# Kernel tuning notes

Measured on AMD Instinct MI355X. Metric: run time of the kernel, lower is better.

Reference implementation:

```python
import jax, jax.numpy as jnp
from jax import lax
import numpy as np

SMOOTH = 0.015
EPS = 1e-9


def setup_inputs() -> dict:
    key = jax.random.key(0)
    k_x, k_a, k_p, k_b = jax.random.split(key, 4)
    B, F, T, C = 64, 256, 2048, 1
    x = jax.random.uniform(k_x, (B, F, T, C), dtype=jnp.float32)  # nonneg energies
    # learned scalars ~ N(1.0, 0.1) as in tf.random_normal_initializer(mean=1.0, stddev=0.1)
    alpha = 1.0 + 0.1 * jax.random.normal(k_a, (1,), dtype=jnp.float32)
    power = 1.0 + 0.1 * jax.random.normal(k_p, (1,), dtype=jnp.float32)
    bias = 1.0 + 0.1 * jax.random.normal(k_b, (1,), dtype=jnp.float32)
    return {"x": x, "alpha": alpha, "power": power, "bias": bias}


def _smoother(x):
    # x: [B, F, T, C]; IIR: M_0 = s*x_0, M_t = (1-s)*M_{t-1} + s*x_t
    xt = jnp.moveaxis(x, 2, 0)  # [T, B, F, C]
    m0 = SMOOTH * xt[0]

    def step(m_prev, xi):
        m = (1.0 - SMOOTH) * m_prev + SMOOTH * xi
        return m, m

    _, ms = lax.scan(step, m0, xt[1:])
    M = jnp.concatenate([m0[None], ms], axis=0)  # [T, B, F, C]
    return jnp.moveaxis(M, 0, 2)  # [B, F, T, C]


def reference(x, alpha, power, bias):
    M = _smoother(x)
    return jnp.power(x / jnp.power(EPS + M, alpha) + bias, power) - jnp.power(bias, power)
```

## Files before the change

kernel.cpp:

```cpp
#include <hip/hip_runtime.h>


#define T_LEN      2048
#define PAD_STRIDE 33
#define LDS_ROW    (64 * PAD_STRIDE)

__device__ __forceinline__ float fast_exp2(float x) { return __builtin_amdgcn_exp2f(x); }
__device__ __forceinline__ float fast_log2(float x) { return __builtin_amdgcn_logf(x); }

__global__ __launch_bounds__(256) void pcen_kernel(
    const float* __restrict__ x,
    const float* __restrict__ alpha_p,
    const float* __restrict__ power_p,
    const float* __restrict__ bias_p,
    float* __restrict__ out)
{
    __shared__ float lds[4][LDS_ROW];

    const int wave = threadIdx.x >> 6;
    const int lane = threadIdx.x & 63;
    const int row  = (blockIdx.x << 2) | wave;

    const float alpha = alpha_p[0];
    const float power = power_p[0];
    const float bias  = bias_p[0];

    const float A = 0.985f;
    const float S = 0.015f;

    const float* xr  = x   + (size_t)row * T_LEN;
    float*       orw = out + (size_t)row * T_LEN;
    float*       L   = lds[wave];

#pragma unroll
    for (int k = 0; k < 8; ++k) {
        const int e = 4 * lane + 256 * k;
        const float4 v = *reinterpret_cast<const float4*>(xr + e);
        const int idx = ((e >> 5) * PAD_STRIDE) + (e & 31);
        L[idx + 0] = v.x; L[idx + 1] = v.y; L[idx + 2] = v.z; L[idx + 3] = v.w;
    }
    __syncthreads();

    float xv[32], mv[32];
    const int base = lane * PAD_STRIDE;
    float m = 0.0f;
#pragma unroll
    for (int j = 0; j < 32; ++j) {
        const float xx = L[base + j];
        xv[j] = xx;
        m = A * m + S * xx;
        mv[j] = m;
    }

    float f = A; f *= f; f *= f; f *= f; f *= f; f *= f;
    float s = m;
    float g = f;
#pragma unroll
    for (int d = 1; d < 64; d <<= 1) {
        const float so = __shfl_up(s, d, 64);
        if (lane >= d) s += g * so;
        g *= g;
    }
    float carry = __shfl_up(s, 1, 64);
    if (lane == 0) carry = 0.0f;

    const float bias_pow = fast_exp2(power * fast_log2(bias));
    float pa = A * carry;
#pragma unroll
    for (int j = 0; j < 32; ++j) {
        const float M   = mv[j] + pa;
        pa *= A;
        const float den = 1e-9f + M;
        const float t   = xv[j] * fast_exp2(-alpha * fast_log2(den)) + bias;
        const float r   = fast_exp2(power * fast_log2(t)) - bias_pow;
        L[base + j] = r;
    }
    __syncthreads();

#pragma unroll
    for (int k = 0; k < 8; ++k) {
        const int e   = 4 * lane + 256 * k;
        const int idx = ((e >> 5) * PAD_STRIDE) + (e & 31);
        float4 v;
        v.x = L[idx + 0]; v.y = L[idx + 1]; v.z = L[idx + 2]; v.w = L[idx + 3];
        *reinterpret_cast<float4*>(orw + e) = v;
    }
}

extern "C" void kernel_launch(void* const* d_in, const int* in_sizes, int n_in,
                              void* d_out, int out_size, void* d_ws, size_t ws_size,
                              hipStream_t stream) {
    const float* x       = (const float*)d_in[0];
    const float* alpha_p = (const float*)d_in[1];
    const float* power_p = (const float*)d_in[2];
    const float* bias_p  = (const float*)d_in[3];
    float* out           = (float*)d_out;

    const int nrows  = in_sizes[0] / T_LEN;
    const int blocks = nrows / 4;

    pcen_kernel<<<blocks, 256, 0, stream>>>(x, alpha_p, power_p, bias_p, out);
}
```

Measured before the change: 237.8 us.

## Replace LDS transpose with chunked register scan and cross-chunk carry

Drops the shared-memory transpose. Each lane now loads 8 contiguous elements per 512-element chunk straight into registers, runs a local recurrence, then a wave-wide shuffle scan with a carry passed between four chunks. Later chunks are prefetched while earlier ones are computed. This removes the LDS traffic and the block barriers and lowers register pressure, allowing higher occupancy (launch bounds 256,8). The cost is more shuffle-scan rounds, four scans instead of one, and narrower per-lane memory accesses.

```diff
diff --git a/kernel.cpp b/kernel.cpp
--- a/kernel.cpp
+++ b/kernel.cpp
@@ -1,22 +1,20 @@
 #include <hip/hip_runtime.h>
 
 
-#define T_LEN      2048
-#define PAD_STRIDE 33
-#define LDS_ROW    (64 * PAD_STRIDE)
+#define T_LEN 2048
+#define CHUNK 512
+#define PLANE 8
 
 __device__ __forceinline__ float fast_exp2(float x) { return __builtin_amdgcn_exp2f(x); }
 __device__ __forceinline__ float fast_log2(float x) { return __builtin_amdgcn_logf(x); }
 
-__global__ __launch_bounds__(256) void pcen_kernel(
+__global__ __launch_bounds__(256, 8) void pcen_kernel(
     const float* __restrict__ x,
     const float* __restrict__ alpha_p,
     const float* __restrict__ power_p,
     const float* __restrict__ bias_p,
     float* __restrict__ out)
 {
-    __shared__ float lds[4][LDS_ROW];
-
     const int wave = threadIdx.x >> 6;
     const int lane = threadIdx.x & 63;
     const int row  = (blockIdx.x << 2) | wave;
@@ -27,64 +25,69 @@
 
     const float A = 0.985f;
     const float S = 0.015f;
+    float f8 = A * A; f8 *= f8; f8 *= f8;
 
-    const float* xr  = x   + (size_t)row * T_LEN;
-    float*       orw = out + (size_t)row * T_LEN;
-    float*       L   = lds[wave];
-
-#pragma unroll
-    for (int k = 0; k < 8; ++k) {
-        const int e = 4 * lane + 256 * k;
-        const float4 v = *reinterpret_cast<const float4*>(xr + e);
-        const int idx = ((e >> 5) * PAD_STRIDE) + (e & 31);
-        L[idx + 0] = v.x; L[idx + 1] = v.y; L[idx + 2] = v.z; L[idx + 3] = v.w;
-    }
-    __syncthreads();
-
-    float xv[32], mv[32];
-    const int base = lane * PAD_STRIDE;
-    float m = 0.0f;
-#pragma unroll
-    for (int j = 0; j < 32; ++j) {
-        const float xx = L[base + j];
-        xv[j] = xx;
-        m = A * m + S * xx;
-        mv[j] = m;
-    }
-
-    float f = A; f *= f; f *= f; f *= f; f *= f; f *= f;
-    float s = m;
-    float g = f;
-#pragma unroll
-    for (int d = 1; d < 64; d <<= 1) {
-        const float so = __shfl_up(s, d, 64);
-        if (lane >= d) s += g * so;
-        g *= g;
-    }
-    float carry = __shfl_up(s, 1, 64);
-    if (lane == 0) carry = 0.0f;
+    const float* xr  = x   + (size_t)row * T_LEN + PLANE * lane;
+    float*       orw = out + (size_t)row * T_LEN + PLANE * lane;
 
     const float bias_pow = fast_exp2(power * fast_log2(bias));
-    float pa = A * carry;
-#pragma unroll
-    for (int j = 0; j < 32; ++j) {
-        const float M   = mv[j] + pa;
-        pa *= A;
-        const float den = 1e-9f + M;
-        const float t   = xv[j] * fast_exp2(-alpha * fast_log2(den)) + bias;
-        const float r   = fast_exp2(power * fast_log2(t)) - bias_pow;
-        L[base + j] = r;
-    }
-    __syncthreads();
+    const float nalpha   = -alpha;
 
-#pragma unroll
-    for (int k = 0; k < 8; ++k) {
-        const int e   = 4 * lane + 256 * k;
-        const int idx = ((e >> 5) * PAD_STRIDE) + (e & 31);
-        float4 v;
-        v.x = L[idx + 0]; v.y = L[idx + 1]; v.z = L[idx + 2]; v.w = L[idx + 3];
-        *reinterpret_cast<float4*>(orw + e) = v;
-    }
+    float carry = 0.0f;
+
+    float4 a0 = *reinterpret_cast<const float4*>(xr + 0 * CHUNK);
+    float4 b0 = *reinterpret_cast<const float4*>(xr + 0 * CHUNK + 4);
+    float4 a1 = *reinterpret_cast<const float4*>(xr + 1 * CHUNK);
+    float4 b1 = *reinterpret_cast<const float4*>(xr + 1 * CHUNK + 4);
+    float4 a2, b2, a3, b3;
+
+#define PROC(cc, va, vb)                                                      \
+  {                                                                           \
+    float xv[PLANE];                                                          \
+    xv[0] = va.x; xv[1] = va.y; xv[2] = va.z; xv[3] = va.w;                   \
+    xv[4] = vb.x; xv[5] = vb.y; xv[6] = vb.z; xv[7] = vb.w;                   \
+    float mv[PLANE];                                                          \
+    float m = 0.0f;                                                           \
+    _Pragma("unroll")                                                         \
+    for (int j = 0; j < PLANE; ++j) { m = A * m + S * xv[j]; mv[j] = m; }     \
+    \
+    \
+    float s = (lane == 0) ? fmaf(f8, carry, m) : m;                           \
+    float g = f8;                                                             \
+    _Pragma("unroll")                                                         \
+    for (int d = 1; d < 64; d <<= 1) {                                        \
+      float so = __shfl_up(s, d, 64);                                         \
+      if (lane >= d) s = fmaf(g, so, s);                                      \
+      g *= g;                                                                 \
+    }                                                                         \
+    float C = __shfl_up(s, 1, 64);     \
+    if (lane == 0) C = carry;                                                 \
+    carry = __shfl(s, 63, 64);          \
+    float pa = A * C;                         \
+    _Pragma("unroll")                                                         \
+    for (int j = 0; j < PLANE; ++j) {                                         \
+      float M   = mv[j] + pa;                                                 \
+      pa *= A;                                                                \
+      float den = 1e-9f + M;                                                  \
+      float t   = fmaf(xv[j], fast_exp2(nalpha * fast_log2(den)), bias);      \
+      xv[j]     = fast_exp2(power * fast_log2(t)) - bias_pow;                 \
+    }                                                                         \
+    float4 w0, w1;                                                            \
+    w0.x = xv[0]; w0.y = xv[1]; w0.z = xv[2]; w0.w = xv[3];                   \
+    w1.x = xv[4]; w1.y = xv[5]; w1.z = xv[6]; w1.w = xv[7];                   \
+    *reinterpret_cast<float4*>(orw + (cc) * CHUNK)     = w0;                  \
+    *reinterpret_cast<float4*>(orw + (cc) * CHUNK + 4) = w1;                  \
+  }
+
+    a2 = *reinterpret_cast<const float4*>(xr + 2 * CHUNK);
+    b2 = *reinterpret_cast<const float4*>(xr + 2 * CHUNK + 4);
+    PROC(0, a0, b0);
+    a3 = *reinterpret_cast<const float4*>(xr + 3 * CHUNK);
+    b3 = *reinterpret_cast<const float4*>(xr + 3 * CHUNK + 4);
+    PROC(1, a1, b1);
+    PROC(2, a2, b2);
+    PROC(3, a3, b3);
+#undef PROC
 }
 
 extern "C" void kernel_launch(void* const* d_in, const int* in_sizes, int n_in,
```

New measurement: 237.2 us. Within noise of the previous version (-0.2%).

## Replace LDS transpose with register-resident chunked scan using cross-chunk carries

Applied to the files above, without the earlier changes.

Drops the shared-memory transpose and the two block barriers. Each lane now keeps its eight float4 loads in registers and runs eight interleaved 64-lane shuffle scans, one per 256-element chunk. Chunks are stitched together with a running carry read from lane 63. This removes LDS traffic and synchronisation, at the cost of more shuffle instructions (eight scans instead of one) and higher register pressure, with an occupancy hint added to the launch bounds.

```diff
diff --git a/kernel.cpp b/kernel.cpp
--- a/kernel.cpp
+++ b/kernel.cpp
@@ -1,22 +1,23 @@
 #include <hip/hip_runtime.h>
 
 
-#define T_LEN      2048
-#define PAD_STRIDE 33
-#define LDS_ROW    (64 * PAD_STRIDE)
+#define T_LEN 2048
+#define NCH   8
+#define CHUNK 256
 
 __device__ __forceinline__ float fast_exp2(float x) { return __builtin_amdgcn_exp2f(x); }
 __device__ __forceinline__ float fast_log2(float x) { return __builtin_amdgcn_logf(x); }
+__device__ __forceinline__ float readlane63(float v) {
+    return __int_as_float(__builtin_amdgcn_readlane(__float_as_int(v), 63));
+}
 
-__global__ __launch_bounds__(256) void pcen_kernel(
+__global__ __launch_bounds__(256, 4) void pcen_kernel(
     const float* __restrict__ x,
     const float* __restrict__ alpha_p,
     const float* __restrict__ power_p,
     const float* __restrict__ bias_p,
     float* __restrict__ out)
 {
-    __shared__ float lds[4][LDS_ROW];
-
     const int wave = threadIdx.x >> 6;
     const int lane = threadIdx.x & 63;
     const int row  = (blockIdx.x << 2) | wave;
@@ -27,63 +28,79 @@
 
     const float A = 0.985f;
     const float S = 0.015f;
+    const float A2 = A * A;
+    const float f4 = A2 * A2;
 
-    const float* xr  = x   + (size_t)row * T_LEN;
-    float*       orw = out + (size_t)row * T_LEN;
-    float*       L   = lds[wave];
+    const float* xr  = x   + (size_t)row * T_LEN + 4 * lane;
+    float*       orw = out + (size_t)row * T_LEN + 4 * lane;
 
+    float4 v[NCH];
 #pragma unroll
-    for (int k = 0; k < 8; ++k) {
-        const int e = 4 * lane + 256 * k;
-        const float4 v = *reinterpret_cast<const float4*>(xr + e);
-        const int idx = ((e >> 5) * PAD_STRIDE) + (e & 31);
-        L[idx + 0] = v.x; L[idx + 1] = v.y; L[idx + 2] = v.z; L[idx + 3] = v.w;
+    for (int c = 0; c < NCH; ++c)
+        v[c] = *reinterpret_cast<const float4*>(xr + c * CHUNK);
+
+    float fl = 1.0f, t = f4;
+#pragma unroll
+    for (int b = 1; b < 64; b <<= 1) {
+        fl = (lane & b) ? fl * t : fl;
+        t *= t;
     }
-    __syncthreads();
+    const float F = t;
 
-    float xv[32], mv[32];
-    const int base = lane * PAD_STRIDE;
-    float m = 0.0f;
+    float s[NCH];
 #pragma unroll
-    for (int j = 0; j < 32; ++j) {
-        const float xx = L[base + j];
-        xv[j] = xx;
-        m = A * m + S * xx;
-        mv[j] = m;
+    for (int c = 0; c < NCH; ++c) {
+        float m = 0.0f;
+        m = fmaf(A, m, S * v[c].x);
+        m = fmaf(A, m, S * v[c].y);
+        m = fmaf(A, m, S * v[c].z);
+        m = fmaf(A, m, S * v[c].w);
+        s[c] = m;
     }
 
-    float f = A; f *= f; f *= f; f *= f; f *= f; f *= f;
-    float s = m;
-    float g = f;
+    {
+        float g = f4;
 #pragma unroll
-    for (int d = 1; d < 64; d <<= 1) {
-        const float so = __shfl_up(s, d, 64);
-        if (lane >= d) s += g * so;
-        g *= g;
+        for (int d = 1; d < 64; d <<= 1) {
+#pragma unroll
+            for (int c = 0; c < NCH; ++c) {
+                const float so = __shfl_up(s[c], d, 64);
+                if (lane >= d) s[c] = fmaf(g, so, s[c]);
+            }
+            g *= g;
+        }
     }
-    float carry = __shfl_up(s, 1, 64);
-    if (lane == 0) carry = 0.0f;
+
+    float e[NCH];
+#pragma unroll
+    for (int c = 0; c < NCH; ++c) {
+        e[c] = __shfl_up(s[c], 1, 64);
+        if (lane == 0) e[c] = 0.0f;
+    }
 
     const float bias_pow = fast_exp2(power * fast_log2(bias));
-    float pa = A * carry;
+    const float nalpha   = -alpha;
+
+    float R = 0.0f;
 #pragma unroll
-    for (int j = 0; j < 32; ++j) {
-        const float M   = mv[j] + pa;
-        pa *= A;
-        const float den = 1e-9f + M;
-        const float t   = xv[j] * fast_exp2(-alpha * fast_log2(den)) + bias;
-        const float r   = fast_exp2(power * fast_log2(t)) - bias_pow;
-        L[base + j] = r;
-    }
-    __syncthreads();
+    for (int c = 0; c < NCH; ++c) {
+        const float s63 = readlane63(s[c]);
+        float M = fmaf(fl, R, e[c]);
+        R = fmaf(F, R, s63);
 
+        float4 r;
 #pragma unroll
-    for (int k = 0; k < 8; ++k) {
-        const int e   = 4 * lane + 256 * k;
-        const int idx = ((e >> 5) * PAD_STRIDE) + (e & 31);
-        float4 v;
-        v.x = L[idx + 0]; v.y = L[idx + 1]; v.z = L[idx + 2]; v.w = L[idx + 3];
-        *reinterpret_cast<float4*>(orw + e) = v;
+        for (int j = 0; j < 4; ++j) {
+            const float xj = (j == 0) ? v[c].x : (j == 1) ? v[c].y
+                           : (j == 2) ? v[c].z : v[c].w;
+            M = fmaf(A, M, S * xj);
+            const float den = 1e-9f + M;
+            const float tt  = fmaf(xj, fast_exp2(nalpha * fast_log2(den)), bias);
+            const float rr  = fast_exp2(power * fast_log2(tt)) - bias_pow;
+            if (j == 0) r.x = rr; else if (j == 1) r.y = rr;
+            else if (j == 2) r.z = rr; else r.w = rr;
+        }
+        *reinterpret_cast<float4*>(orw + c * CHUNK) = r;
     }
 }
 
```

After: 236.0 us. No clear change (-0.8%).
